# Optimization experiments

Measured on AMD Instinct MI355X. Metric: run time of the kernel, lower is better.

## Reference

```python
import jax, jax.numpy as jnp
import numpy as np

HIDDEN = 1024
HEADS = 16
HEAD_DIM = HIDDEN // HEADS


def setup_inputs() -> dict:
    key = jax.random.key(0)
    k_x, k_wq, k_bq, k_wo, k_bo = jax.random.split(key, 5)
    x = jax.random.normal(k_x, (2, 2048, HIDDEN), dtype=jnp.float32)
    s = 1.0 / np.sqrt(HIDDEN)
    W_qkv = jax.random.uniform(k_wq, (HIDDEN, 3 * HIDDEN), jnp.float32, -s, s)
    b_qkv = jax.random.uniform(k_bq, (3 * HIDDEN,), jnp.float32, -s, s)
    W_out = jax.random.uniform(k_wo, (HIDDEN, HIDDEN), jnp.float32, -s, s)
    b_out = jax.random.uniform(k_bo, (HIDDEN,), jnp.float32, -s, s)
    return {"x": x, "W_qkv": W_qkv, "b_qkv": b_qkv, "W_out": W_out, "b_out": b_out}


def reference(x, W_qkv, b_qkv, W_out, b_out):
    B, S, D = x.shape
    qkv = x @ W_qkv + b_qkv                       # [B,S,3D]
    qkv = qkv.reshape(B, S, 3, HEADS, HEAD_DIM)
    qkv = jnp.transpose(qkv, (2, 0, 3, 1, 4))     # [3,B,H,S,Dh]
    q, k, v = qkv[0], qkv[1], qkv[2]
    scores = jnp.einsum("bhsd,bhtd->bhst", q, k) / np.sqrt(HEAD_DIM)
    attn = jax.nn.softmax(scores, axis=-1)        # [B,H,S,S]
    out = jnp.einsum("bhst,bhtd->bhsd", attn, v)  # [B,H,S,Dh]
    out = jnp.transpose(out, (0, 2, 1, 3)).reshape(B, S, D)
    return out @ W_out + b_out
```

## Files before the change

kernel.cpp:

```cpp
#include <hip/hip_runtime.h>
#include <hip/hip_bf16.h>

typedef short short8 __attribute__((ext_vector_type(8)));
typedef short short4_ __attribute__((ext_vector_type(4)));
typedef float float4_ __attribute__((ext_vector_type(4)));
typedef unsigned short ushort_t;
typedef unsigned int uint32_t_;
typedef uint32_t_ uint2v __attribute__((ext_vector_type(2)));
typedef uint32_t_ uint4v __attribute__((ext_vector_type(4)));

#define SCL 0.1803368801111f

__device__ __forceinline__ ushort_t f2bf(float f) {
    uint32_t_ u = __builtin_bit_cast(uint32_t_, f);
    u = (u + 0x7fffu + ((u >> 16) & 1u)) >> 16;
    return (ushort_t)u;
}

__device__ __forceinline__ uint32_t_ pack_bf16(float a, float b) {
    uint32_t_ ua = __builtin_bit_cast(uint32_t_, a) + 0x8000u;
    uint32_t_ ub = __builtin_bit_cast(uint32_t_, b) + 0x8000u;
    return __builtin_amdgcn_perm(ub, ua, 0x07060302);
}

__device__ __forceinline__ float4_ mfma16x16x16_bf16(short4_ a, short4_ b, float4_ c) {
#if __has_builtin(__builtin_amdgcn_mfma_f32_16x16x16bf16_1k)
    return __builtin_amdgcn_mfma_f32_16x16x16bf16_1k(a, b, c, 0, 0, 0);
#else
    asm volatile("v_mfma_f32_16x16x16_bf16 %0, %1, %2, %0" : "+v"(c) : "v"(a), "v"(b));
    return c;
#endif
}

#define MFMA32(a, b, c) __builtin_amdgcn_mfma_f32_16x16x32_bf16(a, b, c, 0, 0, 0)

#define GLD_LDS16(g, l) __builtin_amdgcn_global_load_lds( \
    (const __attribute__((address_space(1))) void*)(g),   \
    (__attribute__((address_space(3))) void*)(l), 16, 0, 0)

__global__ void cvt_bf16_k(const float* __restrict__ in, ushort_t* __restrict__ out, int n) {
    int i = (blockIdx.x * blockDim.x + threadIdx.x) * 4;
    if (i + 3 < n) {
        float4 v = *(const float4*)(in + i);
        uint32_t_ lo = (uint32_t_)f2bf(v.x) | ((uint32_t_)f2bf(v.y) << 16);
        uint32_t_ hi = (uint32_t_)f2bf(v.z) | ((uint32_t_)f2bf(v.w) << 16);
        *(uint2*)(out + i) = make_uint2(lo, hi);
    }
}

__global__ void transpose_bf16_k(const float* __restrict__ in, ushort_t* __restrict__ out,
                                 int K, int N) {
    __shared__ float tile[32][33];
    int n0 = blockIdx.x * 32, k0 = blockIdx.y * 32;
    int tx = threadIdx.x & 31, ty = threadIdx.x >> 5;
    #pragma unroll
    for (int i = 0; i < 32; i += 8)
        tile[ty + i][tx] = in[(size_t)(k0 + ty + i) * N + n0 + tx];
    __syncthreads();
    #pragma unroll
    for (int i = 0; i < 32; i += 8)
        out[(size_t)(n0 + ty + i) * K + k0 + tx] = f2bf(tile[tx][ty + i]);
}

template <int TN, bool QKV_EPI>
__global__ __launch_bounds__(256, 2)
void gemm_dbuf_k(const ushort_t* __restrict__ A, const ushort_t* __restrict__ Bt,
                 const float* __restrict__ bias, void* __restrict__ C,
                 ushort_t* __restrict__ Vt_out, int M, int N, int K) {
    constexpr int NB   = TN / 32;
    constexpr int SETB = 8192 + TN * 64;
    __shared__ char smem[2 * SETB];
    const int tid  = threadIdx.x;
    const int m0   = blockIdx.y * 128;
    const int n0   = blockIdx.x * TN;
    const int w    = tid >> 6;
    const int lane = tid & 63;
    const int wm   = (w >> 1) * 64;
    const int wn   = (w & 1) * (TN / 2);
    const int quad = lane >> 4;
    const int l16  = lane & 15;

    const int sr = 16 * w + (lane >> 2);
    const int sc = ((lane & 3) ^ ((sr >> 1) & 3)) * 8;
    const ushort_t* ag0 = A  + (size_t)(m0 + sr) * K + sc;
    const ushort_t* ag1 = A  + (size_t)(m0 + sr + 64) * K + sc;
    const ushort_t* bg0 = Bt + (size_t)(n0 + sr) * K + sc;
    const ushort_t* bg1 = Bt + (size_t)(n0 + sr + 64) * K + sc;
    char* sA = smem + 1024 * w;
    char* sB = smem + 8192 + 1024 * w;

    int aoff[4], boff[NB];
    #pragma unroll
    for (int i = 0; i < 4; i++) {
        int row = wm + i * 16 + l16;
        aoff[i] = row * 64 + ((quad ^ ((row >> 1) & 3)) * 16);
    }
    #pragma unroll
    for (int i = 0; i < NB; i++) {
        int row = wn + i * 16 + l16;
        boff[i] = 8192 + row * 64 + ((quad ^ ((row >> 1) & 3)) * 16);
    }

    float4_ acc[4][NB] = {};
    const int NIT = K >> 5;

    GLD_LDS16(ag0, sA);
    GLD_LDS16(ag1, sA + 4096);
    GLD_LDS16(bg0, sB);
    if (TN == 128) GLD_LDS16(bg1, sB + 4096);

    for (int it = 0; it < NIT; ++it) {
        __syncthreads();
        if (it + 1 < NIT) {
            const int nk = (it + 1) * 32;
            char* dA = sA + ((it + 1) & 1) * SETB;
            char* dB = sB + ((it + 1) & 1) * SETB;
            GLD_LDS16(ag0 + nk, dA);
            GLD_LDS16(ag1 + nk, dA + 4096);
            GLD_LDS16(bg0 + nk, dB);
            if (TN == 128) GLD_LDS16(bg1 + nk, dB + 4096);
        }
        const char* base = smem + (it & 1) * SETB;
        short8 af[4], bf[NB];
        #pragma unroll
        for (int i = 0; i < 4; i++)  af[i] = *(const short8*)(base + aoff[i]);
        #pragma unroll
        for (int i = 0; i < NB; i++) bf[i] = *(const short8*)(base + boff[i]);
        #pragma unroll
        for (int mi = 0; mi < 4; mi++)
            #pragma unroll
            for (int ni = 0; ni < NB; ni++)
                acc[mi][ni] = MFMA32(af[mi], bf[ni], acc[mi][ni]);
    }

    #pragma unroll
    for (int mi = 0; mi < 4; mi++) {
        int row = m0 + wm + mi * 16 + quad * 4;
        #pragma unroll
        for (int ni = 0; ni < NB; ni++) {
            int col = n0 + wn + ni * 16 + l16;
            float bb = bias[col];
            if (QKV_EPI) {
                if (col < 2048) {
                    float sc2 = (col < 1024) ? SCL : 1.0f;
                    #pragma unroll
                    for (int r = 0; r < 4; r++)
                        ((ushort_t*)C)[(size_t)(row + r) * 2048 + col] =
                            f2bf((acc[mi][ni][r] + bb) * sc2);
                } else {
                    int s0v  = row & 2047;
                    int spos = (s0v & ~31) | (quad << 3) | ((mi & 1) << 2);
                    size_t vrow = (size_t)((row >> 11) * 1024 + (col - 2048));
                    float v0 = acc[mi][ni][0] + bb, v1 = acc[mi][ni][1] + bb;
                    float v2 = acc[mi][ni][2] + bb, v3 = acc[mi][ni][3] + bb;
                    uint2v pk;
                    pk.x = pack_bf16(v0, v1);
                    pk.y = pack_bf16(v2, v3);
                    *(uint2v*)(Vt_out + vrow * 2048 + spos) = pk;
                }
            } else {
                #pragma unroll
                for (int r = 0; r < 4; r++)
                    ((float*)C)[(size_t)(row + r) * N + col] = acc[mi][ni][r] + bb;
            }
        }
    }
}

__global__ __launch_bounds__(256, 4)
void flash_attn_k(const ushort_t* __restrict__ qk, const ushort_t* __restrict__ vt,
                  ushort_t* __restrict__ out) {
    __shared__ char smem[32768];
    const int bh = blockIdx.y;
    const int b  = bh >> 4, h = bh & 15;
    const int q0 = blockIdx.x * 64;
    const int tid  = threadIdx.x;
    const int w    = tid >> 6;
    const int lane = tid & 63;
    const int quad = lane >> 4;
    const int l16  = lane & 15;
    const int qh   = w >> 1;
    const int kh   = w & 1;
    const size_t tok0 = (size_t)b * 2048;
    const int hq = h * 64;

    const int r0 = 16 * w + (lane >> 3), r1 = r0 + 8;
    const int s7 = lane & 7;
    const int c0 = (s7 ^ ((r0 >> 1) & 7)) * 8;
    const int c1 = (s7 ^ ((r1 >> 1) & 7)) * 8;
    const ushort_t* qg0 = qk + (tok0 + q0 + r0) * 2048 + hq + c0;
    const ushort_t* qg1 = qk + (tok0 + q0 + r1) * 2048 + hq + c1;
    const ushort_t* kg0 = qk + (tok0 + r0) * 2048 + 1024 + hq + c0;
    const ushort_t* kg1 = qk + (tok0 + r1) * 2048 + 1024 + hq + c1;
    const ushort_t* vg0 = vt + (size_t)(bh * 64 + r0) * 2048 + c0;
    const ushort_t* vg1 = vt + (size_t)(bh * 64 + r1) * 2048 + c1;
    char* stK = smem + 2048 * w;
    char* stV = smem + 8192 + 2048 * w;
    char* stQ = smem + 16384 + 2048 * w;

    GLD_LDS16(qg0, stQ);
    GLD_LDS16(qg1, stQ + 1024);
    GLD_LDS16(kg0, stK);
    GLD_LDS16(kg1, stK + 1024);
    GLD_LDS16(vg0, stV);
    GLD_LDS16(vg1, stV + 1024);
    __syncthreads();

    const int sw = (l16 >> 1) & 7;
    short8 qf[2][2];
    #pragma unroll
    for (int sub = 0; sub < 2; sub++)
        #pragma unroll
        for (int kk = 0; kk < 2; kk++) {
            int row = qh * 32 + sub * 16 + l16;
            qf[sub][kk] = *(const short8*)(smem + 16384 + row * 128 +
                                           (((kk * 4 + quad) ^ sw) * 16));
        }

    int koff[2][2], voff[4];
    #pragma unroll
    for (int mi = 0; mi < 2; mi++)
        #pragma unroll
        for (int kk = 0; kk < 2; kk++) {
            int row = kh * 32 + mi * 16 + l16;
            koff[mi][kk] = row * 128 + (((kk * 4 + quad) ^ sw) * 16);
        }
    #pragma unroll
    for (int di = 0; di < 4; di++) {
        int row = di * 16 + l16;
        voff[di] = 8192 + row * 128 + (((kh * 4 + quad) ^ sw) * 16);
    }

    float4_ ot[2][4] = {};
    float lsum[2] = {0.f, 0.f};

    for (int kt = 0; kt < 2048; kt += 64) {
        __syncthreads();
        const int set = (kt >> 6) & 1;
        if (kt + 64 < 2048) {
            const int nb = (set ^ 1) * 16384;
            const size_t go = (size_t)(kt + 64);
            GLD_LDS16(kg0 + go * 2048, stK + nb);
            GLD_LDS16(kg1 + go * 2048, stK + nb + 1024);
            GLD_LDS16(vg0 + go, stV + nb);
            GLD_LDS16(vg1 + go, stV + nb + 1024);
        }
        const char* base = smem + set * 16384;

        float4_ st[2][2];
        #pragma unroll
        for (int mi = 0; mi < 2; mi++) {
            short8 kf0 = *(const short8*)(base + koff[mi][0]);
            short8 kf1 = *(const short8*)(base + koff[mi][1]);
            #pragma unroll
            for (int sub = 0; sub < 2; sub++) {
                float4_ z = {0.f, 0.f, 0.f, 0.f};
                z = MFMA32(kf0, qf[sub][0], z);
                z = MFMA32(kf1, qf[sub][1], z);
                st[mi][sub] = z;
            }
        }

        short4_ bp[2][2];
        #pragma unroll
        for (int sub = 0; sub < 2; sub++)
            #pragma unroll
            for (int mi = 0; mi < 2; mi++) {
                float p0 = __builtin_amdgcn_exp2f(st[mi][sub][0]);
                float p1 = __builtin_amdgcn_exp2f(st[mi][sub][1]);
                float p2 = __builtin_amdgcn_exp2f(st[mi][sub][2]);
                float p3 = __builtin_amdgcn_exp2f(st[mi][sub][3]);
                lsum[sub] += (p0 + p1) + (p2 + p3);
                uint2v d;
                d.x = pack_bf16(p0, p1);
                d.y = pack_bf16(p2, p3);
                bp[sub][mi] = __builtin_bit_cast(short4_, d);
            }

        #pragma unroll
        for (int di = 0; di < 4; di++) {
            short8 vv = *(const short8*)(base + voff[di]);
            short4_ av0 = __builtin_shufflevector(vv, vv, 0, 1, 2, 3);
            short4_ av1 = __builtin_shufflevector(vv, vv, 4, 5, 6, 7);
            #pragma unroll
            for (int sub = 0; sub < 2; sub++) {
                ot[sub][di] = mfma16x16x16_bf16(av0, bp[sub][0], ot[sub][di]);
                ot[sub][di] = mfma16x16x16_bf16(av1, bp[sub][1], ot[sub][di]);
            }
        }
    }

    #pragma unroll
    for (int sub = 0; sub < 2; sub++) {
        float t = lsum[sub];
        t += __shfl_xor(t, 16, 64);
        t += __shfl_xor(t, 32, 64);
        lsum[sub] = t;
    }

    float* Obuf = (float*)smem;
    float* lbuf = (float*)(smem + 17408);
    __syncthreads();
    #pragma unroll
    for (int sub = 0; sub < 2; sub++)
        lbuf[(qh * 32 + sub * 16 + l16) * 2 + kh] = lsum[sub];
    if (kh == 1) {
        #pragma unroll
        for (int sub = 0; sub < 2; sub++)
            #pragma unroll
            for (int di = 0; di < 4; di++)
                *(float4_*)&Obuf[(qh * 32 + sub * 16 + l16) * 68 + di * 16 + quad * 4] = ot[sub][di];
    }
    __syncthreads();
    if (kh == 0) {
        #pragma unroll
        for (int sub = 0; sub < 2; sub++)
            #pragma unroll
            for (int di = 0; di < 4; di++) {
                float4_* p = (float4_*)&Obuf[(qh * 32 + sub * 16 + l16) * 68 + di * 16 + quad * 4];
                *p = *p + ot[sub][di];
            }
    }
    __syncthreads();

    {
        int q  = tid >> 2;
        int ds = (tid & 3) * 16;
        float linv = 1.0f / (lbuf[q * 2] + lbuf[q * 2 + 1]);
        const float* ob = &Obuf[q * 68 + ds];
        float4_ v0 = *(const float4_*)(ob);
        float4_ v1 = *(const float4_*)(ob + 4);
        float4_ v2 = *(const float4_*)(ob + 8);
        float4_ v3 = *(const float4_*)(ob + 12);
        uint4v d0, d1;
        d0.x = pack_bf16(v0[0] * linv, v0[1] * linv);
        d0.y = pack_bf16(v0[2] * linv, v0[3] * linv);
        d0.z = pack_bf16(v1[0] * linv, v1[1] * linv);
        d0.w = pack_bf16(v1[2] * linv, v1[3] * linv);
        d1.x = pack_bf16(v2[0] * linv, v2[1] * linv);
        d1.y = pack_bf16(v2[2] * linv, v2[3] * linv);
        d1.z = pack_bf16(v3[0] * linv, v3[1] * linv);
        d1.w = pack_bf16(v3[2] * linv, v3[3] * linv);
        ushort_t* dst = out + (tok0 + q0 + (size_t)q) * 1024 + hq + ds;
        *(uint4v*)(dst)     = d0;
        *(uint4v*)(dst + 8) = d1;
    }
}

extern "C" void kernel_launch(void* const* d_in, const int* in_sizes, int n_in,
                              void* d_out, int out_size, void* d_ws, size_t ws_size,
                              hipStream_t stream) {
    const float* x    = (const float*)d_in[0];
    const float* Wqkv = (const float*)d_in[1];
    const float* bqkv = (const float*)d_in[2];
    const float* Wout = (const float*)d_in[3];
    const float* bout = (const float*)d_in[4];
    float* out = (float*)d_out;

    char* ws = (char*)d_ws;
    ushort_t* x_bf    = (ushort_t*)(ws);
    ushort_t* WqkvT   = (ushort_t*)(ws + 8388608);
    ushort_t* WoutT   = (ushort_t*)(ws + 14680064);
    ushort_t* qk_bf   = (ushort_t*)(ws + 16777216);
    ushort_t* vt_bf   = (ushort_t*)(ws + 33554432);
    ushort_t* attn_bf = (ushort_t*)(ws + 41943040);

    cvt_bf16_k<<<4096, 256, 0, stream>>>(x, x_bf, 4096 * 1024);
    transpose_bf16_k<<<dim3(96, 32), 256, 0, stream>>>(Wqkv, WqkvT, 1024, 3072);
    transpose_bf16_k<<<dim3(32, 32), 256, 0, stream>>>(Wout, WoutT, 1024, 1024);

    gemm_dbuf_k<128, true><<<dim3(24, 32), 256, 0, stream>>>(
        x_bf, WqkvT, bqkv, (void*)qk_bf, vt_bf, 4096, 3072, 1024);

    flash_attn_k<<<dim3(32, 32), 256, 0, stream>>>(qk_bf, vt_bf, attn_bf);

    gemm_dbuf_k<64, false><<<dim3(16, 32), 256, 0, stream>>>(
        attn_bf, WoutT, bout, (void*)out, nullptr, 4096, 1024, 1024);
}
```

Baseline: 187.6 us.

## Fuse prep kernels, raise occupancy bounds, swap attention grid order

Merges the x conversion and both weight transposes into one prep kernel launch that dispatches on block index, removing two kernel launches. Raises the launch_bounds min-blocks hints for the GEMMs and flash attention to push for higher occupancy, which may force register spills. Swaps the flash attention grid so batch-head varies fastest, changing which blocks run together and how K/V are reused in cache.

```diff
diff --git a/kernel.cpp b/kernel.cpp
--- a/kernel.cpp
+++ b/kernel.cpp
@@ -38,21 +38,34 @@
     (const __attribute__((address_space(1))) void*)(g),   \
     (__attribute__((address_space(3))) void*)(l), 16, 0, 0)
 
-__global__ void cvt_bf16_k(const float* __restrict__ in, ushort_t* __restrict__ out, int n) {
-    int i = (blockIdx.x * blockDim.x + threadIdx.x) * 4;
-    if (i + 3 < n) {
-        float4 v = *(const float4*)(in + i);
+__global__ __launch_bounds__(256)
+void prep_k(const float* __restrict__ x, ushort_t* __restrict__ x_bf,
+            const float* __restrict__ Wqkv, ushort_t* __restrict__ WqkvT,
+            const float* __restrict__ Wout, ushort_t* __restrict__ WoutT) {
+    __shared__ float tile[32][33];
+    const int id = blockIdx.x;
+    const int tid = threadIdx.x;
+    if (id < 4096) {
+        int i = (id * 256 + tid) * 4;
+        float4 v = *(const float4*)(x + i);
         uint32_t_ lo = (uint32_t_)f2bf(v.x) | ((uint32_t_)f2bf(v.y) << 16);
         uint32_t_ hi = (uint32_t_)f2bf(v.z) | ((uint32_t_)f2bf(v.w) << 16);
-        *(uint2*)(out + i) = make_uint2(lo, hi);
-    }
-}
-
-__global__ void transpose_bf16_k(const float* __restrict__ in, ushort_t* __restrict__ out,
-                                 int K, int N) {
-    __shared__ float tile[32][33];
-    int n0 = blockIdx.x * 32, k0 = blockIdx.y * 32;
-    int tx = threadIdx.x & 31, ty = threadIdx.x >> 5;
+        *(uint2*)(x_bf + i) = make_uint2(lo, hi);
+        return;
+    }
+    const float* in;
+    ushort_t* out;
+    int N, K, n0, k0;
+    if (id < 7168) {
+        int t = id - 4096;
+        in = Wqkv; out = WqkvT; N = 3072; K = 1024;
+        n0 = (t % 96) * 32; k0 = (t / 96) * 32;
+    } else {
+        int t = id - 7168;
+        in = Wout; out = WoutT; N = 1024; K = 1024;
+        n0 = (t & 31) * 32; k0 = (t >> 5) * 32;
+    }
+    int tx = tid & 31, ty = tid >> 5;
     #pragma unroll
     for (int i = 0; i < 32; i += 8)
         tile[ty + i][tx] = in[(size_t)(k0 + ty + i) * N + n0 + tx];
@@ -63,7 +76,7 @@
 }
 
 template <int TN, bool QKV_EPI>
-__global__ __launch_bounds__(256, 2)
+__global__ __launch_bounds__(256, TN == 128 ? 3 : 4)
 void gemm_dbuf_k(const ushort_t* __restrict__ A, const ushort_t* __restrict__ Bt,
                  const float* __restrict__ bias, void* __restrict__ C,
                  ushort_t* __restrict__ Vt_out, int M, int N, int K) {
@@ -167,13 +180,13 @@
     }
 }
 
-__global__ __launch_bounds__(256, 4)
+__global__ __launch_bounds__(256, 5)
 void flash_attn_k(const ushort_t* __restrict__ qk, const ushort_t* __restrict__ vt,
                   ushort_t* __restrict__ out) {
     __shared__ char smem[32768];
-    const int bh = blockIdx.y;
+    const int bh = blockIdx.x;
     const int b  = bh >> 4, h = bh & 15;
-    const int q0 = blockIdx.x * 64;
+    const int q0 = blockIdx.y * 64;
     const int tid  = threadIdx.x;
     const int w    = tid >> 6;
     const int lane = tid & 63;
@@ -365,9 +378,7 @@
     ushort_t* vt_bf   = (ushort_t*)(ws + 33554432);
     ushort_t* attn_bf = (ushort_t*)(ws + 41943040);
 
-    cvt_bf16_k<<<4096, 256, 0, stream>>>(x, x_bf, 4096 * 1024);
-    transpose_bf16_k<<<dim3(96, 32), 256, 0, stream>>>(Wqkv, WqkvT, 1024, 3072);
-    transpose_bf16_k<<<dim3(32, 32), 256, 0, stream>>>(Wout, WoutT, 1024, 1024);
+    prep_k<<<8192, 256, 0, stream>>>(x, x_bf, Wqkv, WqkvT, Wout, WoutT);
 
     gemm_dbuf_k<128, true><<<dim3(24, 32), 256, 0, stream>>>(
         x_bf, WqkvT, bqkv, (void*)qk_bf, vt_bf, 4096, 3072, 1024);
```

Result: faster. 182.8 us (-2.6%).
